# Optimization experiments

Hardware: AMD Instinct MI355X
Metric: run time of the kernel (lower is better)

The kernel has to match this reference:

```python
import jax, jax.numpy as jnp
import numpy as np

B, C, D, H, W = 2, 64, 3, 96, 96
CD = C * D  # conv1x1 channel count = in_dim * 3


def setup_inputs() -> dict:
    key = jax.random.key(0)
    ks = jax.random.split(key, 7)
    s = 1.0 / np.sqrt(CD)
    x = jax.random.normal(ks[0], (B, C, D, H, W), dtype=jnp.float32)
    Wq = jax.random.uniform(ks[1], (CD, CD), jnp.float32, -s, s)
    bq = jax.random.uniform(ks[2], (CD,), jnp.float32, -s, s)
    Wk = jax.random.uniform(ks[3], (CD, CD), jnp.float32, -s, s)
    bk = jax.random.uniform(ks[4], (CD,), jnp.float32, -s, s)
    Wv = jax.random.uniform(ks[5], (CD, CD), jnp.float32, -s, s)
    bv = jax.random.uniform(ks[6], (CD,), jnp.float32, -s, s)
    return {"x": x, "Wq": Wq, "bq": bq, "Wk": Wk, "bk": bk, "Wv": Wv, "bv": bv}


def reference(x, Wq, bq, Wk, bk, Wv, bv):
    b, c, d, h, w = x.shape
    n = h * w
    xr = x.reshape(b, c * d, n)  # [B, CD, N]; conv1x1 == channel matmul
    q = jnp.einsum('oc,bcn->bon', Wq, xr) + bq[:, None]  # [B, CD, N]
    k = jnp.einsum('oc,bcn->bon', Wk, xr) + bk[:, None]
    v = jnp.einsum('oc,bcn->bon', Wv, xr) + bv[:, None]
    energy = jnp.einsum('bcn,bcm->bnm', q, k)            # [B, N, N]
    attention = jax.nn.softmax(energy, axis=-1)
    # out = bmm(value, attention^T): out[b,c,m] = sum_n v[b,c,n] * attn[b,m,n]
    out = jnp.einsum('bcn,bmn->bcm', v, attention)       # [B, CD, N]
    return out.reshape(b, c, d, h, w)
```

## Files before the change

kernel.cpp:

```cpp
#include <hip/hip_runtime.h>

#define NSEQ  9216
#define CDIM  192
#define LOG2E 1.44269504088896f

typedef _Float16 h8_t  __attribute__((ext_vector_type(8)));
typedef _Float16 h4_t  __attribute__((ext_vector_type(4)));
typedef _Float16 h2_t  __attribute__((ext_vector_type(2)));
typedef __fp16   fp16x2 __attribute__((ext_vector_type(2)));
typedef float    f4_t  __attribute__((ext_vector_type(4)));
typedef float    f16v  __attribute__((ext_vector_type(16)));
typedef unsigned u32x2 __attribute__((ext_vector_type(2)));

static __device__ inline unsigned f2u(float f) { union { float f; unsigned u; } x; x.f = f; return x.u; }
static __device__ inline float u2f(unsigned u) { union { unsigned u; float f; } x; x.u = u; return x.f; }

static __device__ inline unsigned cvt_pk(float a, float b) {
    union { fp16x2 h; unsigned u; } x;
    x.h = __builtin_amdgcn_cvt_pkrtz(a, b);
    return x.u;
}

static __device__ inline u32x2 plswap(unsigned a, unsigned b) {
    return __builtin_amdgcn_permlane32_swap(a, b, false, false);
}

__global__ __launch_bounds__(256) void wconv_kernel(
    const float* __restrict__ Wq, const float* __restrict__ Wk,
    const float* __restrict__ Wv, _Float16* __restrict__ Wh)
{
    int i = blockIdx.x * 256 + threadIdx.x;
    if (i >= 3 * 9216) return;
    const float* src = (i < 9216) ? Wq : (i < 18432 ? Wk : Wv);
    float s = (i < 9216) ? LOG2E : 1.f;
    int r = i % 9216;
    f4_t w = ((const f4_t*)src)[r];
    h4_t h = {(_Float16)(w[0]*s), (_Float16)(w[1]*s),
              (_Float16)(w[2]*s), (_Float16)(w[3]*s)};
    ((h4_t*)Wh)[i] = h;
}

__global__ __launch_bounds__(256) void proj_kernel(
    const float* __restrict__ x, const _Float16* __restrict__ Wh,
    const float* __restrict__ bq, const float* __restrict__ bk,
    const float* __restrict__ bv,
    _Float16* __restrict__ QT, _Float16* __restrict__ KT, _Float16* __restrict__ Vg)
{
    const int tid  = threadIdx.x;
    const int lane = tid & 63, wave = tid >> 6;
    const int L31  = lane & 31, hi = lane >> 5;
    const int idx  = blockIdx.x * 4 + wave;
    const int mat  = idx / 576;
    const int rem  = idx % 576;
    const int b    = rem / 288;
    const int n0   = (rem % 288) * 32;
    const int n    = n0 + L31;

    h8_t bf[12];
    #pragma unroll
    for (int t = 0; t < 12; t++) {
        h8_t h;
        #pragma unroll
        for (int j = 0; j < 8; j++)
            h[j] = (_Float16)x[(size_t)(b * CDIM + t * 16 + hi * 8 + j) * NSEQ + n];
        bf[t] = h;
    }

    const _Float16* W = Wh + mat * CDIM * CDIM;
    const float* bias = (mat == 0) ? bq : (mat == 1 ? bk : bv);
    const float bscale = (mat == 0) ? LOG2E : 1.f;

    f16v acc[6];
    #pragma unroll
    for (int s = 0; s < 6; s++)
        #pragma unroll
        for (int r = 0; r < 16; r++) acc[s][r] = 0.f;

    #pragma unroll
    for (int t = 0; t < 12; t++) {
        #pragma unroll
        for (int s = 0; s < 6; s++) {
            h8_t a = *(const h8_t*)(W + (s * 32 + L31) * CDIM + t * 16 + hi * 8);
            acc[s] = __builtin_amdgcn_mfma_f32_32x32x16_f16(a, bf[t], acc[s], 0, 0, 0);
        }
    }

    if (mat < 2) {
        _Float16* dst = ((mat == 0) ? QT : KT) + ((size_t)b * NSEQ + n) * CDIM;
        #pragma unroll
        for (int s = 0; s < 6; s++) {
            #pragma unroll
            for (int g = 0; g < 4; g++) {
                f4_t bb = *(const f4_t*)&bias[s * 32 + 8 * g + 4 * hi];
                h4_t h = {(_Float16)(acc[s][4*g+0] + bb[0] * bscale),
                          (_Float16)(acc[s][4*g+1] + bb[1] * bscale),
                          (_Float16)(acc[s][4*g+2] + bb[2] * bscale),
                          (_Float16)(acc[s][4*g+3] + bb[3] * bscale)};
                *(h4_t*)(dst + s * 32 + 8 * g + 4 * hi) = h;
            }
        }
    } else {
        #pragma unroll
        for (int s = 0; s < 6; s++) {
            #pragma unroll
            for (int g = 0; g < 4; g++) {
                f4_t bb = *(const f4_t*)&bias[s * 32 + 8 * g + 4 * hi];
                #pragma unroll
                for (int r = 0; r < 4; r++) {
                    int o = s * 32 + 8 * g + 4 * hi + r;
                    Vg[((size_t)b * CDIM + o) * NSEQ + n] =
                        (_Float16)(acc[s][4*g+r] + bb[r]);
                }
            }
        }
    }
}

template<int NSPLIT>
__global__ __launch_bounds__(256, 2) void flash_kernel(
    const _Float16* __restrict__ QT, const _Float16* __restrict__ KTg,
    const _Float16* __restrict__ Vg,
    _Float16* __restrict__ O_part, float* __restrict__ m_part, float* __restrict__ l_part)
{
    constexpr int KPS    = NSEQ / NSPLIT;
    constexpr int KITERS = KPS / 32;
    constexpr int KBUF   = 32 * 200;
    constexpr int DBUF   = 14080;
    __shared__ __align__(16) _Float16 Sh[2 * DBUF];

    const int tid  = threadIdx.x;
    const int lane = tid & 63, wave = tid >> 6;
    const int L31  = lane & 31, hi = lane >> 5;
    const int qtile = blockIdx.x, split = blockIdx.y, b = blockIdx.z;
    const int q0 = qtile * 128 + wave * 32;

    h8_t qf[12];
    const _Float16* qbase = QT + ((size_t)b * NSEQ + q0 + L31) * CDIM + hi * 8;
    #pragma unroll
    for (int t = 0; t < 12; t++) qf[t] = *(const h8_t*)(qbase + t * 16);

    f16v acc[6];
    #pragma unroll
    for (int s = 0; s < 6; s++)
        #pragma unroll
        for (int r = 0; r < 16; r++) acc[s][r] = 0.f;
    float m_run = -__builtin_inff();
    float l_run = 0.f;

    const _Float16* ksrc = KTg + ((size_t)b * NSEQ + split * KPS) * CDIM;
    const _Float16* vsrc = Vg + (size_t)b * CDIM * NSEQ + split * KPS;

    int kds[3], vds[3];
    const _Float16 *kgl[3], *vgl[3];
    #pragma unroll
    for (int r = 0; r < 3; r++) {
        int i = r * 256 + tid;
        kds[r] = (i / 24) * 200 + (i % 24) * 8;
        kgl[r] = ksrc + i * 8;
        int c = i >> 2, seg = i & 3;
        vds[r] = KBUF + c * 40 + seg * 8;
        vgl[r] = vsrc + (size_t)c * NSEQ + seg * 8;
    }

    h8_t kreg[3], vreg[3];
    #pragma unroll
    for (int r = 0; r < 3; r++) kreg[r] = *(const h8_t*)(kgl[r]);
    #pragma unroll
    for (int r = 0; r < 3; r++) vreg[r] = *(const h8_t*)(vgl[r]);
    #pragma unroll
    for (int r = 0; r < 3; r++) *(h8_t*)(Sh + kds[r]) = kreg[r];
    #pragma unroll
    for (int r = 0; r < 3; r++) *(h8_t*)(Sh + vds[r]) = vreg[r];
    if (KITERS > 1) {
        #pragma unroll
        for (int r = 0; r < 3; r++) kreg[r] = *(const h8_t*)(kgl[r] + 32 * CDIM);
        #pragma unroll
        for (int r = 0; r < 3; r++) vreg[r] = *(const h8_t*)(vgl[r] + 32);
    }
    __syncthreads();

    for (int kt = 0; kt < KITERS; kt++) {
        const int rb = (kt & 1) * DBUF;
        const int wb = ((kt + 1) & 1) * DBUF;

        if (kt + 1 < KITERS) {
            #pragma unroll
            for (int r = 0; r < 3; r++) *(h8_t*)(Sh + wb + kds[r]) = kreg[r];
            #pragma unroll
            for (int r = 0; r < 3; r++) *(h8_t*)(Sh + wb + vds[r]) = vreg[r];
        }
        if (kt + 2 < KITERS) {
            #pragma unroll
            for (int r = 0; r < 3; r++)
                kreg[r] = *(const h8_t*)(kgl[r] + (kt + 2) * 32 * CDIM);
            #pragma unroll
            for (int r = 0; r < 3; r++)
                vreg[r] = *(const h8_t*)(vgl[r] + (kt + 2) * 32);
        }

        f16v st;
        #pragma unroll
        for (int r = 0; r < 16; r++) st[r] = 0.f;
        #pragma unroll
        for (int t = 0; t < 12; t++) {
            h8_t a = *(const h8_t*)(Sh + rb + L31 * 200 + t * 16 + hi * 8);
            st = __builtin_amdgcn_mfma_f32_32x32x16_f16(a, qf[t], st, 0, 0, 0);
        }

        float a0 = fmaxf(fmaxf(st[0], st[1]),  st[2]);
        float a1 = fmaxf(fmaxf(st[3], st[4]),  st[5]);
        float a2 = fmaxf(fmaxf(st[6], st[7]),  st[8]);
        float a3 = fmaxf(fmaxf(st[9], st[10]), st[11]);
        float a4 = fmaxf(fmaxf(st[12], st[13]), st[14]);
        float mx = fmaxf(fmaxf(fmaxf(a0, a1), fmaxf(a2, a3)), fmaxf(a4, st[15]));
        u32x2 mxw = plswap(f2u(mx), f2u(mx));
        mx = fmaxf(u2f(mxw[0]), u2f(mxw[1]));

        if (__builtin_expect(__any(mx > m_run + 9.f), 0)) {
            float m_new = fmaxf(m_run, mx);
            float alpha = __builtin_exp2f(m_run - m_new);
            l_run *= alpha;
            #pragma unroll
            for (int cs = 0; cs < 6; cs++)
                #pragma unroll
                for (int r = 0; r < 16; r++) acc[cs][r] *= alpha;
            m_run = m_new;
        }

        unsigned pu[8];
        float ps0 = 0.f, ps1 = 0.f;
        #pragma unroll
        for (int t2 = 0; t2 < 8; t2++) {
            float e0 = __builtin_exp2f(st[2*t2]   - m_run);
            float e1 = __builtin_exp2f(st[2*t2+1] - m_run);
            ps0 += e0; ps1 += e1;
            pu[t2] = cvt_pk(e0, e1);
        }
        l_run += ps0 + ps1;

        union { h8_t h; unsigned u[4]; } pb0, pb1;
        u32x2 x0 = plswap(pu[0], pu[2]);
        u32x2 x1 = plswap(pu[1], pu[3]);
        u32x2 x2 = plswap(pu[4], pu[6]);
        u32x2 x3 = plswap(pu[5], pu[7]);
        pb0.u[0] = x0[0]; pb0.u[1] = x1[0]; pb0.u[2] = x0[1]; pb0.u[3] = x1[1];
        pb1.u[0] = x2[0]; pb1.u[1] = x3[0]; pb1.u[2] = x2[1]; pb1.u[3] = x3[1];

        #pragma unroll
        for (int ks = 0; ks < 2; ks++) {
            h8_t pb = ks ? pb1.h : pb0.h;
            #pragma unroll
            for (int cs = 0; cs < 6; cs++) {
                h8_t va = *(const h8_t*)(Sh + rb + KBUF + (cs * 32 + L31) * 40 + ks * 16 + hi * 8);
                acc[cs] = __builtin_amdgcn_mfma_f32_32x32x16_f16(va, pb, acc[cs], 0, 0, 0);
            }
        }

        __syncthreads();
    }

    u32x2 lw = plswap(f2u(l_run), f2u(l_run));
    float l_tot = u2f(lw[0]) + u2f(lw[1]);
    const size_t pw = (size_t)(b * NSPLIT + split) * NSEQ + q0;
    if (lane < 32) {
        m_part[pw + lane] = m_run;
        l_part[pw + lane] = l_tot;
    }
    _Float16* T = Sh + wave * 6400;
    #pragma unroll
    for (int cs = 0; cs < 6; cs++)
        #pragma unroll
        for (int g = 0; g < 4; g++) {
            h4_t hh = {(_Float16)acc[cs][4*g+0], (_Float16)acc[cs][4*g+1],
                       (_Float16)acc[cs][4*g+2], (_Float16)acc[cs][4*g+3]};
            *(h4_t*)(T + L31 * 200 + cs * 32 + 8 * g + 4 * hi) = hh;
        }
    _Float16* ob = O_part + pw * CDIM;
    #pragma unroll
    for (int it = 0; it < 12; it++) {
        int i = it * 64 + lane;
        int qq = i / 24, col = i % 24;
        h8_t h = *(const h8_t*)(T + qq * 200 + col * 8);
        *(h8_t*)(ob + (size_t)qq * CDIM + col * 8) = h;
    }
}

template<int NS>
__global__ __launch_bounds__(256) void combine_kernel(
    const _Float16* __restrict__ O_part, const float* __restrict__ m_part,
    const float* __restrict__ l_part, float* __restrict__ out)
{
    __shared__ float Cs[CDIM][33];
    __shared__ float winv[NS][32];
    const int tid = threadIdx.x;
    const int b  = blockIdx.y;
    const int n0 = blockIdx.x * 32;

    if (tid < 32) {
        int n = n0 + tid;
        float mm[NS], ll[NS], ms = -__builtin_inff();
        #pragma unroll
        for (int s = 0; s < NS; s++) {
            mm[s] = m_part[(b * NS + s) * NSEQ + n];
            ll[s] = l_part[(b * NS + s) * NSEQ + n];
            ms = fmaxf(ms, mm[s]);
        }
        float denom = 0.f;
        #pragma unroll
        for (int s = 0; s < NS; s++) {
            float w = __builtin_exp2f(mm[s] - ms);
            mm[s] = w;
            denom += w * ll[s];
        }
        #pragma unroll
        for (int s = 0; s < NS; s++) winv[s][tid] = mm[s] / denom;
    }
    __syncthreads();

    for (int i = tid; i < 32 * 96; i += 256) {
        int nl = i / 96, cp = i % 96;
        float v0 = 0.f, v1 = 0.f;
        #pragma unroll
        for (int s = 0; s < NS; s++) {
            h2_t op = *(const h2_t*)(O_part +
                ((size_t)(b * NS + s) * NSEQ + n0 + nl) * CDIM + cp * 2);
            float w = winv[s][nl];
            v0 += w * (float)op[0];
            v1 += w * (float)op[1];
        }
        Cs[cp * 2][nl] = v0;
        Cs[cp * 2 + 1][nl] = v1;
    }
    __syncthreads();
    for (int i = tid; i < CDIM * 32; i += 256) {
        int nl = i & 31, c = i >> 5;
        out[((size_t)b * CDIM + c) * NSEQ + n0 + nl] = Cs[c][nl];
    }
}

extern "C" void kernel_launch(void* const* d_in, const int* in_sizes, int n_in,
                              void* d_out, int out_size, void* d_ws, size_t ws_size,
                              hipStream_t stream)
{
    const float* x  = (const float*)d_in[0];
    const float* Wq = (const float*)d_in[1];
    const float* bq = (const float*)d_in[2];
    const float* Wk = (const float*)d_in[3];
    const float* bk = (const float*)d_in[4];
    const float* Wv = (const float*)d_in[5];
    const float* bv = (const float*)d_in[6];
    float* out = (float*)d_out;

    char* ws = (char*)d_ws;
    _Float16* QT = (_Float16*)(ws);
    _Float16* KT = (_Float16*)(ws + 7077888);
    _Float16* Vg = (_Float16*)(ws + 14155776);
    char* tail = ws + 21233664;
    _Float16* Wh = (_Float16*)tail;
    _Float16* O_part = (_Float16*)tail;

    wconv_kernel<<<108, 256, 0, stream>>>(Wq, Wk, Wv, Wh);
    proj_kernel<<<432, 256, 0, stream>>>(x, Wh, bq, bk, bv, QT, KT, Vg);

    const size_t need8 = 21233664ull + 8 * 7077888ull + 2 * 589824ull;
    const size_t need4 = 21233664ull + 4 * 7077888ull + 2 * 294912ull;
    if (ws_size >= need8) {
        float* m_part = (float*)(tail + 8 * 7077888ull);
        float* l_part = (float*)(tail + 8 * 7077888ull + 589824ull);
        flash_kernel<8><<<dim3(72, 8, 2), 256, 0, stream>>>(QT, KT, Vg, O_part, m_part, l_part);
        combine_kernel<8><<<dim3(288, 2), 256, 0, stream>>>(O_part, m_part, l_part, out);
    } else if (ws_size >= need4) {
        float* m_part = (float*)(tail + 4 * 7077888ull);
        float* l_part = (float*)(tail + 4 * 7077888ull + 294912ull);
        flash_kernel<4><<<dim3(72, 4, 2), 256, 0, stream>>>(QT, KT, Vg, O_part, m_part, l_part);
        combine_kernel<4><<<dim3(288, 2), 256, 0, stream>>>(O_part, m_part, l_part, out);
    } else {
        float* m_part = (float*)(tail + 2 * 7077888ull);
        float* l_part = (float*)(tail + 2 * 7077888ull + 147456ull);
        flash_kernel<2><<<dim3(72, 2, 2), 256, 0, stream>>>(QT, KT, Vg, O_part, m_part, l_part);
        combine_kernel<2><<<dim3(288, 2), 256, 0, stream>>>(O_part, m_part, l_part, out);
    }
}
```

Before: 283.0 us.

## Share x tile via LDS in projection, add MFMA priority, vectorize combine loads

```diff
diff --git a/kernel.cpp b/kernel.cpp
--- a/kernel.cpp
+++ b/kernel.cpp
@@ -40,74 +40,89 @@
     ((h4_t*)Wh)[i] = h;
 }
 
-__global__ __launch_bounds__(256) void proj_kernel(
+__global__ __launch_bounds__(384) void proj_kernel(
     const float* __restrict__ x, const _Float16* __restrict__ Wh,
     const float* __restrict__ bq, const float* __restrict__ bk,
     const float* __restrict__ bv,
     _Float16* __restrict__ QT, _Float16* __restrict__ KT, _Float16* __restrict__ Vg)
 {
+    __shared__ __align__(16) _Float16 Xs[32 * 200];
+
     const int tid  = threadIdx.x;
     const int lane = tid & 63, wave = tid >> 6;
     const int L31  = lane & 31, hi = lane >> 5;
-    const int idx  = blockIdx.x * 4 + wave;
-    const int mat  = idx / 576;
-    const int rem  = idx % 576;
-    const int b    = rem / 288;
-    const int n0   = (rem % 288) * 32;
-    const int n    = n0 + L31;
+    const int b    = blockIdx.x / 288;
+    const int n0   = (blockIdx.x % 288) * 32;
+
+    {
+        const int nn = tid & 31;
+        const int c0 = (tid >> 5) * 16;
+        const float* xp = x + (size_t)(b * CDIM + c0) * NSEQ + n0 + nn;
+        _Float16 tmp[16];
+        #pragma unroll
+        for (int j = 0; j < 16; j++)
+            tmp[j] = (_Float16)xp[(size_t)j * NSEQ];
+        #pragma unroll
+        for (int g = 0; g < 4; g++) {
+            h4_t h = {tmp[4*g], tmp[4*g+1], tmp[4*g+2], tmp[4*g+3]};
+            *(h4_t*)(Xs + nn * 200 + c0 + 4 * g) = h;
+        }
+    }
+    __syncthreads();
+
+    const int mat = wave >> 1;
+    const int sh  = (wave & 1) * 3;
+    const int n   = n0 + L31;
 
     h8_t bf[12];
     #pragma unroll
-    for (int t = 0; t < 12; t++) {
-        h8_t h;
-        #pragma unroll
-        for (int j = 0; j < 8; j++)
-            h[j] = (_Float16)x[(size_t)(b * CDIM + t * 16 + hi * 8 + j) * NSEQ + n];
-        bf[t] = h;
-    }
+    for (int t = 0; t < 12; t++)
+        bf[t] = *(const h8_t*)(Xs + L31 * 200 + t * 16 + hi * 8);
 
     const _Float16* W = Wh + mat * CDIM * CDIM;
     const float* bias = (mat == 0) ? bq : (mat == 1 ? bk : bv);
     const float bscale = (mat == 0) ? LOG2E : 1.f;
 
-    f16v acc[6];
-    #pragma unroll
-    for (int s = 0; s < 6; s++)
+    f16v acc[3];
+    #pragma unroll
+    for (int s = 0; s < 3; s++)
         #pragma unroll
         for (int r = 0; r < 16; r++) acc[s][r] = 0.f;
 
+    __builtin_amdgcn_s_setprio(1);
     #pragma unroll
     for (int t = 0; t < 12; t++) {
         #pragma unroll
-        for (int s = 0; s < 6; s++) {
-            h8_t a = *(const h8_t*)(W + (s * 32 + L31) * CDIM + t * 16 + hi * 8);
+        for (int s = 0; s < 3; s++) {
+            h8_t a = *(const h8_t*)(W + ((sh + s) * 32 + L31) * CDIM + t * 16 + hi * 8);
             acc[s] = __builtin_amdgcn_mfma_f32_32x32x16_f16(a, bf[t], acc[s], 0, 0, 0);
         }
     }
+    __builtin_amdgcn_s_setprio(0);
 
     if (mat < 2) {
         _Float16* dst = ((mat == 0) ? QT : KT) + ((size_t)b * NSEQ + n) * CDIM;
         #pragma unroll
-        for (int s = 0; s < 6; s++) {
+        for (int s = 0; s < 3; s++) {
             #pragma unroll
             for (int g = 0; g < 4; g++) {
-                f4_t bb = *(const f4_t*)&bias[s * 32 + 8 * g + 4 * hi];
+                f4_t bb = *(const f4_t*)&bias[(sh + s) * 32 + 8 * g + 4 * hi];
                 h4_t h = {(_Float16)(acc[s][4*g+0] + bb[0] * bscale),
                           (_Float16)(acc[s][4*g+1] + bb[1] * bscale),
                           (_Float16)(acc[s][4*g+2] + bb[2] * bscale),
                           (_Float16)(acc[s][4*g+3] + bb[3] * bscale)};
-                *(h4_t*)(dst + s * 32 + 8 * g + 4 * hi) = h;
+                *(h4_t*)(dst + (sh + s) * 32 + 8 * g + 4 * hi) = h;
             }
         }
     } else {
         #pragma unroll
-        for (int s = 0; s < 6; s++) {
+        for (int s = 0; s < 3; s++) {
             #pragma unroll
             for (int g = 0; g < 4; g++) {
-                f4_t bb = *(const f4_t*)&bias[s * 32 + 8 * g + 4 * hi];
+                f4_t bb = *(const f4_t*)&bias[(sh + s) * 32 + 8 * g + 4 * hi];
                 #pragma unroll
                 for (int r = 0; r < 4; r++) {
-                    int o = s * 32 + 8 * g + 4 * hi + r;
+                    int o = (sh + s) * 32 + 8 * g + 4 * hi + r;
                     Vg[((size_t)b * CDIM + o) * NSEQ + n] =
                         (_Float16)(acc[s][4*g+r] + bb[r]);
                 }
@@ -201,11 +216,13 @@
         f16v st;
         #pragma unroll
         for (int r = 0; r < 16; r++) st[r] = 0.f;
+        __builtin_amdgcn_s_setprio(1);
         #pragma unroll
         for (int t = 0; t < 12; t++) {
             h8_t a = *(const h8_t*)(Sh + rb + L31 * 200 + t * 16 + hi * 8);
             st = __builtin_amdgcn_mfma_f32_32x32x16_f16(a, qf[t], st, 0, 0, 0);
         }
+        __builtin_amdgcn_s_setprio(0);
 
         float a0 = fmaxf(fmaxf(st[0], st[1]),  st[2]);
         float a1 = fmaxf(fmaxf(st[3], st[4]),  st[5]);
@@ -246,6 +263,7 @@
         pb0.u[0] = x0[0]; pb0.u[1] = x1[0]; pb0.u[2] = x0[1]; pb0.u[3] = x1[1];
         pb1.u[0] = x2[0]; pb1.u[1] = x3[0]; pb1.u[2] = x2[1]; pb1.u[3] = x3[1];
 
+        __builtin_amdgcn_s_setprio(1);
         #pragma unroll
         for (int ks = 0; ks < 2; ks++) {
             h8_t pb = ks ? pb1.h : pb0.h;
@@ -255,6 +273,7 @@
                 acc[cs] = __builtin_amdgcn_mfma_f32_32x32x16_f16(va, pb, acc[cs], 0, 0, 0);
             }
         }
+        __builtin_amdgcn_s_setprio(0);
 
         __syncthreads();
     }
@@ -317,19 +336,21 @@
     }
     __syncthreads();
 
-    for (int i = tid; i < 32 * 96; i += 256) {
-        int nl = i / 96, cp = i % 96;
-        float v0 = 0.f, v1 = 0.f;
+    for (int i = tid; i < 32 * 24; i += 256) {
+        int nl = i / 24, cp = i % 24;
+        float v[8];
+        #pragma unroll
+        for (int j = 0; j < 8; j++) v[j] = 0.f;
         #pragma unroll
         for (int s = 0; s < NS; s++) {
-            h2_t op = *(const h2_t*)(O_part +
-                ((size_t)(b * NS + s) * NSEQ + n0 + nl) * CDIM + cp * 2);
+            h8_t op = *(const h8_t*)(O_part +
+                ((size_t)(b * NS + s) * NSEQ + n0 + nl) * CDIM + cp * 8);
             float w = winv[s][nl];
-            v0 += w * (float)op[0];
-            v1 += w * (float)op[1];
-        }
-        Cs[cp * 2][nl] = v0;
-        Cs[cp * 2 + 1][nl] = v1;
+            #pragma unroll
+            for (int j = 0; j < 8; j++) v[j] += w * (float)op[j];
+        }
+        #pragma unroll
+        for (int j = 0; j < 8; j++) Cs[cp * 8 + j][nl] = v[j];
     }
     __syncthreads();
     for (int i = tid; i < CDIM * 32; i += 256) {
@@ -360,7 +381,7 @@
     _Float16* O_part = (_Float16*)tail;
 
     wconv_kernel<<<108, 256, 0, stream>>>(Wq, Wk, Wv, Wh);
-    proj_kernel<<<432, 256, 0, stream>>>(x, Wh, bq, bk, bv, QT, KT, Vg);
+    proj_kernel<<<576, 384, 0, stream>>>(x, Wh, bq, bk, bv, QT, KT, Vg);
 
     const size_t need8 = 21233664ull + 8 * 7077888ull + 2 * 589824ull;
     const size_t need4 = 21233664ull + 4 * 7077888ull + 2 * 294912ull;
```

Measured after the change: 299.8 us. 5.9% more time.
